# Performance work log

Measured on AMD Instinct MI355X. Metric: run time of the kernel, lower is better.

The kernel has to match this reference:

```python
import jax, jax.numpy as jnp
import numpy as np

D_MODEL = 512
D_INNER = 1024  # expand * d_model
D_STATE = 128
D_CONV = 4
DT_RANK = 32
DT_MIN, DT_MAX, DT_FLOOR = 0.001, 0.1, 1e-4


def setup_inputs() -> dict:
    key = jax.random.key(0)
    ks = jax.random.split(key, 8)
    B, S = 2, 1024
    return {
        "x": jax.random.normal(ks[0], (B, S, D_MODEL), jnp.float32),
        "W_in": jax.random.normal(ks[1], (D_MODEL, 2 * D_INNER), jnp.float32) * 0.02,
        "conv_w": jax.random.normal(ks[2], (D_INNER, 1, D_CONV), jnp.float32) * 0.1,
        "conv_b": jnp.zeros((D_INNER,), jnp.float32),
        "W_x": jax.random.normal(ks[3], (D_INNER, DT_RANK + 2 * D_STATE), jnp.float32) * 0.02,
        "W_dt": jax.random.normal(ks[4], (DT_RANK, D_INNER), jnp.float32) * 0.02,
        "b_dt": jnp.zeros((D_INNER,), jnp.float32),
        "W_out": jax.random.normal(ks[5], (D_INNER, D_MODEL), jnp.float32) * 0.02,
    }


def _mamba_forward(x, W_in, conv_w, conv_b, W_x, W_dt, b_dt, W_out):
    Bsz, S, _ = x.shape
    xr = x @ W_in                              # [B,S,2*d_inner]
    xs, res = jnp.split(xr, 2, axis=-1)        # each [B,S,d_inner]

    # depthwise causal conv (torch pads both sides by d_conv-1 then truncates
    # to seq_len, which equals a left-pad-only causal conv)
    xc = xs.transpose(0, 2, 1)                 # [B,d_inner,S]
    xc = jax.lax.conv_general_dilated(
        xc, conv_w, window_strides=(1,), padding=[(D_CONV - 1, 0)],
        feature_group_count=D_INNER)
    u = (xc + conv_b[None, :, None]).transpose(0, 2, 1)  # [B,S,d_inner]

    dbl = u @ W_x                              # [B,S,dt_rank+2*d_state]
    dt, Bm, Cm = jnp.split(dbl, [DT_RANK, DT_RANK + D_STATE], axis=-1)
    dt = dt @ W_dt + b_dt                      # [B,S,d_inner]
    dt = jnp.clip(jax.nn.softplus(dt + DT_FLOOR), DT_MIN, DT_MAX)

    # selective scan: h_t = h_{t-1}*(1-dt_t) + x_t (outer) B_t ; y_t = h_t . C_t
    def step(h, inp):
        x_t, dt_t, B_t, C_t = inp              # [B,d_inner],[B,d_inner],[B,N],[B,N]
        h = h * (1.0 - dt_t)[..., None] + x_t[..., None] * B_t[:, None, :]
        y = jnp.einsum('bdn,bn->bd', h, C_t)
        return h, y

    h0 = jnp.zeros((Bsz, D_INNER, D_STATE), u.dtype)
    xs_t = (u.transpose(1, 0, 2), dt.transpose(1, 0, 2),
            Bm.transpose(1, 0, 2), Cm.transpose(1, 0, 2))
    _, ys = jax.lax.scan(step, h0, xs_t)       # ys: [S,B,d_inner]

    y = ys.transpose(1, 0, 2) + res
    return y @ W_out                           # [B,S,d_model]


def reference(x, W_in, conv_w, conv_b, W_x, W_dt, b_dt, W_out):
    return _mamba_forward(x, W_in, conv_w, conv_b, W_x, W_dt, b_dt, W_out)
```

## Files before the change

### kernel.cpp

```cpp
#include <hip/hip_runtime.h>
#include <math.h>

#define S_LEN 1024
#define BATCH 2
#define DM 512
#define DI 1024
#define DS 128
#define DTR 32
#define CL 64
#define NC (S_LEN / CL)

typedef unsigned short ushortT;
typedef __attribute__((ext_vector_type(8))) short short8;
typedef __attribute__((ext_vector_type(4))) float f32x4;

__device__ __forceinline__ ushortT f2b(float f) {
  unsigned u = __builtin_bit_cast(unsigned, f);
  unsigned r = (u + 0x7fff + ((u >> 16) & 1)) >> 16;
  return (ushortT)r;
}
__device__ __forceinline__ float b2f(ushortT h) {
  return __builtin_bit_cast(float, (unsigned)h << 16);
}

#define GLOAD16(g, l)                                                     \
  __builtin_amdgcn_global_load_lds(                                       \
      (const __attribute__((address_space(1))) void*)(g),                 \
      (__attribute__((address_space(3))) void*)(l), 16, 0, 0)

template<int MODE>
__global__ __launch_bounds__(256) void gemm64(
    const ushortT* __restrict__ A, const ushortT* __restrict__ Bt,
    void* __restrict__ Cout, int N, int K, int ldc, int nbx) {
  __shared__ ushortT As[2][64 * 32];
  __shared__ ushortT Bs[2][64 * 32];
  const int nwg = gridDim.x;
  const int bid = blockIdx.x;
  const int flat = (bid & 7) * (nwg >> 3) + (bid >> 3);
  const int bxi = flat % nbx, byi = flat / nbx;
  const int bm = byi * 64, bn = bxi * 64;
  const int tid = threadIdx.x;
  const int l = tid & 63, w = tid >> 6;
  const int wr = w >> 1, wc = w & 1;
  const int srow = tid >> 2, scol = (tid & 3) * 8;
  const ushortT* gA = A + (size_t)(bm + srow) * K + scol;
  const ushortT* gB = Bt + (size_t)(bn + srow) * K + scol;
  f32x4 acc[2][2] = {};
  const int nt = K >> 5;
  GLOAD16(gA, &As[0][(size_t)tid * 8]);
  GLOAD16(gB, &Bs[0][(size_t)tid * 8]);
  __syncthreads();
  int cur = 0;
  for (int t = 0; t < nt; ++t) {
    if (t + 1 < nt) {
      GLOAD16(gA + (t + 1) * 32, &As[cur ^ 1][(size_t)tid * 8]);
      GLOAD16(gB + (t + 1) * 32, &Bs[cur ^ 1][(size_t)tid * 8]);
    }
    short8 a[2], b[2];
#pragma unroll
    for (int m = 0; m < 2; ++m)
      a[m] = *(const short8*)&As[cur][(wr * 32 + m * 16 + (l & 15)) * 32 + (l >> 4) * 8];
#pragma unroll
    for (int n = 0; n < 2; ++n)
      b[n] = *(const short8*)&Bs[cur][(wc * 32 + n * 16 + (l & 15)) * 32 + (l >> 4) * 8];
#pragma unroll
    for (int m = 0; m < 2; ++m)
#pragma unroll
      for (int n = 0; n < 2; ++n)
        acc[m][n] = __builtin_amdgcn_mfma_f32_16x16x32_bf16(a[m], b[n], acc[m][n], 0, 0, 0);
    __syncthreads();
    cur ^= 1;
  }
#pragma unroll
  for (int m = 0; m < 2; ++m) {
    int grow = bm + wr * 32 + m * 16 + (l >> 4) * 4;
#pragma unroll
    for (int n = 0; n < 2; ++n) {
      int gcol = bn + wc * 32 + n * 16 + (l & 15);
      if (gcol >= N) continue;
#pragma unroll
      for (int i = 0; i < 4; ++i) {
        float v = acc[m][n][i];
        if (MODE == 1)
          ((ushortT*)Cout)[(size_t)(grow + i) * ldc + gcol] = f2b(v);
        else
          ((float*)Cout)[(size_t)(grow + i) * ldc + gcol] = v;
      }
    }
  }
}

__global__ __launch_bounds__(256) void prep_all(
    const float* __restrict__ W_in, const float* __restrict__ W_x,
    const float* __restrict__ W_out, const float* __restrict__ x,
    ushortT* __restrict__ Wt_in, ushortT* __restrict__ Wt_x,
    ushortT* __restrict__ Wt_out, ushortT* __restrict__ x_bf) {
  __shared__ float tb[32][33];
  int bid = blockIdx.x;
  int tx = threadIdx.x, ty = threadIdx.y;
  const float* in; ushortT* out; int K, N, bx, by;
  if (bid < 1024)      { in = W_in;  out = Wt_in;  K = 512;  N = 2048; bx = bid & 63; by = bid >> 6; }
  else if (bid < 1408) { int t2 = bid - 1024; in = W_x;   out = Wt_x;   K = 1024; N = 288;  bx = t2 % 12; by = t2 / 12; }
  else if (bid < 1920) { int t2 = bid - 1408; in = W_out; out = Wt_out; K = 1024; N = 512;  bx = t2 % 16; by = t2 / 16; }
  else {
    int i = (bid - 1920) * 256 + ty * 32 + tx;
    float4 v = ((const float4*)x)[i];
    ushort4 o; o.x = f2b(v.x); o.y = f2b(v.y); o.z = f2b(v.z); o.w = f2b(v.w);
    ((ushort4*)x_bf)[i] = o;
    return;
  }
  int n0 = bx * 32, k0 = by * 32;
  int flat = ty * 32 + tx;
  int r = flat >> 3, c4 = (flat & 7) * 4;
  if (n0 < N) {
#pragma unroll
    for (int i = 0; i < 4; ++i)
      tb[ty + 8 * i][tx] = in[(size_t)(k0 + ty + 8 * i) * N + n0 + tx];
    __syncthreads();
    ushort4 o;
    o.x = f2b(tb[c4][r]);
    o.y = f2b(tb[c4 + 1][r]);
    o.z = f2b(tb[c4 + 2][r]);
    o.w = f2b(tb[c4 + 3][r]);
    *(ushort4*)&out[(size_t)(n0 + r) * K + k0 + c4] = o;
  } else {
    ushort4 z; z.x = 0; z.y = 0; z.z = 0; z.w = 0;
    *(ushort4*)&out[(size_t)(n0 + r) * K + k0 + c4] = z;
  }
}

__global__ __launch_bounds__(256) void conv_kernel(
    const ushortT* __restrict__ xr, const float* __restrict__ w,
    const float* __restrict__ b, ushortT* __restrict__ u) {
  int idx = blockIdx.x * blockDim.x + threadIdx.x;
  int g = idx & 255;
  int s = (idx >> 8) & (S_LEN - 1);
  int bb = idx >> 18;
  int d = g * 4;
  float4 bias = *(const float4*)&b[d];
  float4 w0 = *(const float4*)&w[(d + 0) * 4];
  float4 w1 = *(const float4*)&w[(d + 1) * 4];
  float4 w2 = *(const float4*)&w[(d + 2) * 4];
  float4 w3 = *(const float4*)&w[(d + 3) * 4];
  float a0 = bias.x, a1 = bias.y, a2 = bias.z, a3 = bias.w;
  const ushortT* xs = xr + (size_t)(bb * S_LEN) * (2 * DI) + d;
#pragma unroll
  for (int k = 0; k < 4; ++k) {
    int si = s - 3 + k;
    if (si >= 0) {
      ushort4 v = *(const ushort4*)&xs[(size_t)si * (2 * DI)];
      float wk0 = ((const float*)&w0)[k], wk1 = ((const float*)&w1)[k];
      float wk2 = ((const float*)&w2)[k], wk3 = ((const float*)&w3)[k];
      a0 = fmaf(b2f(v.x), wk0, a0);
      a1 = fmaf(b2f(v.y), wk1, a1);
      a2 = fmaf(b2f(v.z), wk2, a2);
      a3 = fmaf(b2f(v.w), wk3, a3);
    }
  }
  ushort4 o; o.x = f2b(a0); o.y = f2b(a1); o.z = f2b(a2); o.w = f2b(a3);
  *(ushort4*)&u[(size_t)idx * 4] = o;
}

__global__ __launch_bounds__(256) void megachunk(
    const float* __restrict__ dbl, const float* __restrict__ W_dt,
    const float* __restrict__ b_dt, const ushortT* __restrict__ u_bf,
    ushortT* __restrict__ D, ushortT* __restrict__ ut,
    ushortT* __restrict__ zb) {
  __shared__ ushortT Btl[128][72];
  __shared__ float   Dl[64][66];
  __shared__ ushortT utl[64][72];
  __shared__ float   dtl[64][36];
  __shared__ ushortT Wl[32][68];
  const int t = threadIdx.x;
  const int dg = blockIdx.x, bc = blockIdx.y;
  const int b = bc >> 4, c = bc & 15;
  const size_t rowbase = (size_t)(b * S_LEN + c * CL) * DI + dg * 64;

#pragma unroll
  for (int j = 0; j < 8; ++j) {
    int idx4 = j * 256 + t;
    int s = idx4 >> 5, n4 = (idx4 & 31) * 4;
    float4 v = *(const float4*)&dbl[(size_t)(bc * 64 + s) * 288 + 32 + n4];
    Btl[n4][s] = f2b(v.x); Btl[n4 + 1][s] = f2b(v.y);
    Btl[n4 + 2][s] = f2b(v.z); Btl[n4 + 3][s] = f2b(v.w);
  }
#pragma unroll
  for (int j = 0; j < 2; ++j) {
    int idx4 = j * 256 + t;
    int s = idx4 >> 3, k4 = (idx4 & 7) * 4;
    *(float4*)&dtl[s][k4] = *(const float4*)&dbl[(size_t)(bc * 64 + s) * 288 + k4];
  }
#pragma unroll
  for (int j = 0; j < 4; ++j) {
    int idx2 = j * 256 + t;
    int k = idx2 >> 5, d2 = (idx2 & 31) * 2;
    float2 v = *(const float2*)&W_dt[(size_t)k * DI + dg * 64 + d2];
    Wl[k][d2] = f2b(v.x); Wl[k][d2 + 1] = f2b(v.y);
  }
  __syncthreads();

  {
    int d = t & 63, sq = t >> 6;
    float wreg[32];
#pragma unroll
    for (int k = 0; k < 32; ++k) wreg[k] = b2f(Wl[k][d]);
    float bias = b_dt[dg * 64 + d] + 1e-4f;
#pragma unroll 4
    for (int j = 0; j < 16; ++j) {
      int s = sq * 16 + j;
      float acc = bias;
#pragma unroll
      for (int k = 0; k < 32; ++k) acc = fmaf(dtl[s][k], wreg[k], acc);
      acc = (acc > 20.f) ? acc : log1pf(expf(acc));
      acc = fminf(fmaxf(acc, 0.001f), 0.1f);
      Dl[d][s] = 1.f - acc;
    }
  }
  __syncthreads();

  if (t < 64) {
    float cum = 1.f;
#pragma unroll 16
    for (int s = 0; s < CL; ++s) { cum *= Dl[t][s]; Dl[t][s] = cum; }
  }
  __syncthreads();

#pragma unroll
  for (int j = 0; j < 2; ++j) {
    int idx8 = j * 256 + t;
    int s = idx8 >> 3, d8 = (idx8 & 7) * 8;
    float4 raw = *(const float4*)&u_bf[rowbase + (size_t)s * DI + d8];
    const ushortT* up = (const ushortT*)&raw;
#pragma unroll
    for (int k = 0; k < 8; ++k)
      utl[d8 + k][s] = f2b(b2f(up[k]) / Dl[d8 + k][s]);
  }
  __syncthreads();

  {
    const int l = t & 63, w = t >> 6;
    f32x4 acc[8] = {};
#pragma unroll
    for (int kk = 0; kk < 2; ++kk) {
      short8 a = *(const short8*)&utl[w * 16 + (l & 15)][kk * 32 + (l >> 4) * 8];
#pragma unroll
      for (int n = 0; n < 8; ++n) {
        short8 bb = *(const short8*)&Btl[n * 16 + (l & 15)][kk * 32 + (l >> 4) * 8];
        acc[n] = __builtin_amdgcn_mfma_f32_16x16x32_bf16(a, bb, acc[n], 0, 0, 0);
      }
    }
#pragma unroll
    for (int n = 0; n < 8; ++n) {
      int gn = n * 16 + (l & 15);
#pragma unroll
      for (int i = 0; i < 4; ++i) {
        int d = dg * 64 + w * 16 + (l >> 4) * 4 + i;
        zb[(((size_t)(b * NC + c)) * DI + d) * 128 + gn] = f2b(acc[n][i]);
      }
    }
  }

#pragma unroll
  for (int j = 0; j < 2; ++j) {
    int idx8 = j * 256 + t;
    int s = idx8 >> 3, d8 = (idx8 & 7) * 8;
    float4 v; ushortT* vp = (ushortT*)&v;
#pragma unroll
    for (int k = 0; k < 8; ++k) vp[k] = f2b(Dl[d8 + k][s]);
    *(float4*)&D[rowbase + (size_t)s * DI + d8] = v;
  }
#pragma unroll
  for (int j = 0; j < 2; ++j) {
    int idx8 = j * 256 + t;
    int d = idx8 >> 3, s8 = (idx8 & 7) * 8;
    float4 v; ushortT* vp = (ushortT*)&v;
#pragma unroll
    for (int k = 0; k < 8; ++k) vp[k] = utl[d][s8 + k];
    *(float4*)&ut[((size_t)bc * DI + dg * 64 + d) * CL + s8] = v;
  }
}

__global__ __launch_bounds__(256) void scan_pass2(
    const ushortT* __restrict__ zb, const ushortT* __restrict__ D,
    ushortT* __restrict__ hstb) {
  int wid = (blockIdx.x * blockDim.x + threadIdx.x) >> 6;
  int lane = threadIdx.x & 63;
  int b = wid >> 10, d = wid & (DI - 1);
  float h0 = 0.f, h1 = 0.f;
#pragma unroll
  for (int c = 0; c < NC; ++c) {
    float dend = b2f(D[((size_t)(b * S_LEN + c * CL + CL - 1)) * DI + d]);
    size_t addr = (((size_t)(b * NC + c)) * DI + d) * 128 + 2 * lane;
    ushort2 z2 = *(const ushort2*)&zb[addr];
    ushort2 he;
    he.x = f2b(h0); he.y = f2b(h1);
    *(ushort2*)&hstb[addr] = he;
    h0 = dend * (h0 + b2f(z2.x));
    h1 = dend * (h1 + b2f(z2.y));
  }
}

__global__ __launch_bounds__(256) void gemm_y(
    const float* __restrict__ dbl, const ushortT* __restrict__ ut,
    const ushortT* __restrict__ hstb, const ushortT* __restrict__ D,
    const ushortT* __restrict__ xr_bf, ushortT* __restrict__ yr) {
  __shared__ ushortT Bl[64][136];
  __shared__ ushortT Cl[64][136];
  __shared__ ushortT Gl[64][72];
  __shared__ ushortT Ul[64][72];
  __shared__ ushortT Hl[64][136];
  __shared__ ushortT Dl2[64][72];
  const int tid = threadIdx.x;
  const int l = tid & 63, w = tid >> 6;
  const int bc = blockIdx.y, d0 = blockIdx.x * 64;
  const int b = bc >> 4, c = bc & 15;
  const int brow = b * S_LEN + c * CL;
#pragma unroll
  for (int j = 0; j < 2; ++j) {
    int idx4 = j * 256 + tid;
    int dr = idx4 >> 3, s8 = (idx4 & 7) * 8;
    float4 v = *(const float4*)&ut[((size_t)bc * DI + d0 + dr) * CL + s8];
    *(float4*)&Ul[dr][s8] = v;
  }
#pragma unroll
  for (int j = 0; j < 4; ++j) {
    int idx4 = j * 256 + tid;
    int dr = idx4 >> 4, n8 = (idx4 & 15) * 8;
    float4 v = *(const float4*)&hstb[(((size_t)(b * NC + c)) * DI + d0 + dr) * 128 + n8];
    *(float4*)&Hl[dr][n8] = v;
  }
#pragma unroll
  for (int j = 0; j < 2; ++j) {
    int idx4 = j * 256 + tid;
    int tr = idx4 >> 3, d8 = (idx4 & 7) * 8;
    float4 v = *(const float4*)&D[((size_t)(brow + tr)) * DI + d0 + d8];
    *(float4*)&Dl2[tr][d8] = v;
  }
#pragma unroll
  for (int j = 0; j < 16; ++j) {
    int idx4 = j * 256 + tid;
    int row = idx4 >> 6, c4 = (idx4 & 63) * 4;
    float4 v = *(const float4*)&dbl[(size_t)(bc * 64 + row) * 288 + 32 + c4];
    ushortT o0 = f2b(v.x), o1 = f2b(v.y), o2 = f2b(v.z), o3 = f2b(v.w);
    if (c4 < 128) { Bl[row][c4] = o0; Bl[row][c4+1] = o1; Bl[row][c4+2] = o2; Bl[row][c4+3] = o3; }
    else { int cc = c4 - 128; Cl[row][cc] = o0; Cl[row][cc+1] = o1; Cl[row][cc+2] = o2; Cl[row][cc+3] = o3; }
  }
  __syncthreads();
  {
    f32x4 gacc[4] = {};
#pragma unroll
    for (int kk = 0; kk < 4; ++kk) {
      short8 a = *(const short8*)&Cl[w * 16 + (l & 15)][kk * 32 + (l >> 4) * 8];
#pragma unroll
      for (int nf = 0; nf < 4; ++nf) {
        short8 bb = *(const short8*)&Bl[nf * 16 + (l & 15)][kk * 32 + (l >> 4) * 8];
        gacc[nf] = __builtin_amdgcn_mfma_f32_16x16x32_bf16(a, bb, gacc[nf], 0, 0, 0);
      }
    }
#pragma unroll
    for (int nf = 0; nf < 4; ++nf) {
      int s = nf * 16 + (l & 15);
#pragma unroll
      for (int i = 0; i < 4; ++i) {
        int tr = w * 16 + (l >> 4) * 4 + i;
        Gl[tr][s] = f2b((s <= tr) ? gacc[nf][i] : 0.f);
      }
    }
  }
  __syncthreads();
  f32x4 acc[4] = {};
#pragma unroll
  for (int kk = 0; kk < 2; ++kk) {
    short8 a = *(const short8*)&Gl[w * 16 + (l & 15)][kk * 32 + (l >> 4) * 8];
#pragma unroll
    for (int n = 0; n < 4; ++n) {
      short8 bb = *(const short8*)&Ul[n * 16 + (l & 15)][kk * 32 + (l >> 4) * 8];
      acc[n] = __builtin_amdgcn_mfma_f32_16x16x32_bf16(a, bb, acc[n], 0, 0, 0);
    }
  }
#pragma unroll
  for (int kk = 0; kk < 4; ++kk) {
    short8 a = *(const short8*)&Cl[w * 16 + (l & 15)][kk * 32 + (l >> 4) * 8];
#pragma unroll
    for (int n = 0; n < 4; ++n) {
      short8 bb = *(const short8*)&Hl[n * 16 + (l & 15)][kk * 32 + (l >> 4) * 8];
      acc[n] = __builtin_amdgcn_mfma_f32_16x16x32_bf16(a, bb, acc[n], 0, 0, 0);
    }
  }
#pragma unroll
  for (int n = 0; n < 4; ++n) {
    int dl = n * 16 + (l & 15);
    int d = d0 + dl;
#pragma unroll
    for (int i = 0; i < 4; ++i) {
      int tl = w * 16 + (l >> 4) * 4 + i;
      int gr = brow + tl;
      float Dv = b2f(Dl2[tl][dl]);
      float res = b2f(xr_bf[(size_t)gr * 2048 + 1024 + d]);
      yr[(size_t)gr * DI + d] = f2b(acc[n][i] * Dv + res);
    }
  }
}

extern "C" void kernel_launch(void* const* d_in, const int* in_sizes, int n_in,
                              void* d_out, int out_size, void* d_ws, size_t ws_size,
                              hipStream_t stream) {
  const float* x      = (const float*)d_in[0];
  const float* W_in   = (const float*)d_in[1];
  const float* conv_w = (const float*)d_in[2];
  const float* conv_b = (const float*)d_in[3];
  const float* W_x    = (const float*)d_in[4];
  const float* W_dt   = (const float*)d_in[5];
  const float* b_dt   = (const float*)d_in[6];
  const float* W_out  = (const float*)d_in[7];
  float* out = (float*)d_out;
  float* ws = (float*)d_ws;

  ushortT* xr_bf = (ushortT*)ws;
  ushortT* u_bf  = (ushortT*)(ws + 2097152);
  float*   dbl   = ws + 3145728;
  ushortT* Dc    = (ushortT*)(ws + 3735552);
  ushortT* ut    = (ushortT*)(ws + 5832704);
  ushortT* zb    = (ushortT*)(ws + 6881280);
  ushortT* hstb  = (ushortT*)(ws + 8978432);
  ushortT* x_bf  = (ushortT*)(ws + 11075584);
  ushortT* Wt_in = (ushortT*)(ws + 11599872);
  ushortT* Wt_x  = (ushortT*)(ws + 12124160);
  ushortT* Wt_out= (ushortT*)(ws + 12320768);
  ushortT* yr_bf = (ushortT*)(ws + 12582912);

  dim3 blk(256);
  prep_all<<<2944, dim3(32, 8), 0, stream>>>(W_in, W_x, W_out, x,
                                             Wt_in, Wt_x, Wt_out, x_bf);
  gemm64<1><<<1024, blk, 0, stream>>>(x_bf, Wt_in, xr_bf, 2 * DI, DM, 2 * DI, 32);
  conv_kernel<<<2048, blk, 0, stream>>>(xr_bf, conv_w, conv_b, u_bf);
  gemm64<0><<<160, blk, 0, stream>>>(u_bf, Wt_x, dbl, DTR + 2 * DS, DI, DTR + 2 * DS, 5);
  megachunk<<<dim3(16, 32), blk, 0, stream>>>(dbl, W_dt, b_dt, u_bf, Dc, ut, zb);
  scan_pass2<<<512, blk, 0, stream>>>(zb, Dc, hstb);
  gemm_y<<<dim3(16, 32), blk, 0, stream>>>(dbl, ut, hstb, Dc, xr_bf, yr_bf);
  gemm64<0><<<256, blk, 0, stream>>>(yr_bf, Wt_out, out, DM, DI, DM, 8);
}
```

Measured before the change: 94.28 us.

## Fuse inter-chunk state scan into gemm_y by recomputing prefix per block

```diff
diff --git a/kernel.cpp b/kernel.cpp
--- a/kernel.cpp
+++ b/kernel.cpp
@@ -280,29 +280,9 @@
   }
 }
 
-__global__ __launch_bounds__(256) void scan_pass2(
-    const ushortT* __restrict__ zb, const ushortT* __restrict__ D,
-    ushortT* __restrict__ hstb) {
-  int wid = (blockIdx.x * blockDim.x + threadIdx.x) >> 6;
-  int lane = threadIdx.x & 63;
-  int b = wid >> 10, d = wid & (DI - 1);
-  float h0 = 0.f, h1 = 0.f;
-#pragma unroll
-  for (int c = 0; c < NC; ++c) {
-    float dend = b2f(D[((size_t)(b * S_LEN + c * CL + CL - 1)) * DI + d]);
-    size_t addr = (((size_t)(b * NC + c)) * DI + d) * 128 + 2 * lane;
-    ushort2 z2 = *(const ushort2*)&zb[addr];
-    ushort2 he;
-    he.x = f2b(h0); he.y = f2b(h1);
-    *(ushort2*)&hstb[addr] = he;
-    h0 = dend * (h0 + b2f(z2.x));
-    h1 = dend * (h1 + b2f(z2.y));
-  }
-}
-
 __global__ __launch_bounds__(256) void gemm_y(
     const float* __restrict__ dbl, const ushortT* __restrict__ ut,
-    const ushortT* __restrict__ hstb, const ushortT* __restrict__ D,
+    const ushortT* __restrict__ zb, const ushortT* __restrict__ D,
     const ushortT* __restrict__ xr_bf, ushortT* __restrict__ yr) {
   __shared__ ushortT Bl[64][136];
   __shared__ ushortT Cl[64][136];
@@ -315,19 +295,34 @@
   const int bc = blockIdx.y, d0 = blockIdx.x * 64;
   const int b = bc >> 4, c = bc & 15;
   const int brow = b * S_LEN + c * CL;
+
+  {
+    float h[32];
+#pragma unroll
+    for (int i = 0; i < 32; ++i) h[i] = 0.f;
+    const int dth = tid >> 2;
+    for (int cp = 0; cp < c; ++cp) {
+      float dd = b2f(D[((size_t)(b * S_LEN + cp * CL + CL - 1)) * DI + d0 + dth]);
+      const float4* zp = (const float4*)&zb[(((size_t)(b * NC + cp)) * DI + d0) * 128 + (size_t)tid * 32];
+#pragma unroll
+      for (int j = 0; j < 4; ++j) {
+        float4 zv = zp[j];
+        const ushortT* zs = (const ushortT*)&zv;
+#pragma unroll
+        for (int k = 0; k < 8; ++k)
+          h[j * 8 + k] = dd * (h[j * 8 + k] + b2f(zs[k]));
+      }
+    }
+    const int nb = (tid & 3) * 32;
+#pragma unroll
+    for (int i = 0; i < 32; ++i) Hl[dth][nb + i] = f2b(h[i]);
+  }
 #pragma unroll
   for (int j = 0; j < 2; ++j) {
     int idx4 = j * 256 + tid;
     int dr = idx4 >> 3, s8 = (idx4 & 7) * 8;
     float4 v = *(const float4*)&ut[((size_t)bc * DI + d0 + dr) * CL + s8];
     *(float4*)&Ul[dr][s8] = v;
-  }
-#pragma unroll
-  for (int j = 0; j < 4; ++j) {
-    int idx4 = j * 256 + tid;
-    int dr = idx4 >> 4, n8 = (idx4 & 15) * 8;
-    float4 v = *(const float4*)&hstb[(((size_t)(b * NC + c)) * DI + d0 + dr) * 128 + n8];
-    *(float4*)&Hl[dr][n8] = v;
   }
 #pragma unroll
   for (int j = 0; j < 2; ++j) {
@@ -422,7 +417,6 @@
   ushortT* Dc    = (ushortT*)(ws + 3735552);
   ushortT* ut    = (ushortT*)(ws + 5832704);
   ushortT* zb    = (ushortT*)(ws + 6881280);
-  ushortT* hstb  = (ushortT*)(ws + 8978432);
   ushortT* x_bf  = (ushortT*)(ws + 11075584);
   ushortT* Wt_in = (ushortT*)(ws + 11599872);
   ushortT* Wt_x  = (ushortT*)(ws + 12124160);
@@ -436,7 +430,6 @@
   conv_kernel<<<2048, blk, 0, stream>>>(xr_bf, conv_w, conv_b, u_bf);
   gemm64<0><<<160, blk, 0, stream>>>(u_bf, Wt_x, dbl, DTR + 2 * DS, DI, DTR + 2 * DS, 5);
   megachunk<<<dim3(16, 32), blk, 0, stream>>>(dbl, W_dt, b_dt, u_bf, Dc, ut, zb);
-  scan_pass2<<<512, blk, 0, stream>>>(zb, Dc, hstb);
-  gemm_y<<<dim3(16, 32), blk, 0, stream>>>(dbl, ut, hstb, Dc, xr_bf, yr_bf);
+  gemm_y<<<dim3(16, 32), blk, 0, stream>>>(dbl, ut, zb, Dc, xr_bf, yr_bf);
   gemm64<0><<<256, blk, 0, stream>>>(yr_bf, Wt_out, out, DM, DI, DM, 8);
 }
```

New measurement: 94.82 us. No clear change (+0.6%).
